# Performance work log

Hardware: AMD Instinct MI355X
Metric: run time of the kernel (lower is better)

The kernel has to match this reference:

```python
import jax, jax.numpy as jnp
import numpy as np

B, L, D = 8, 8192, 1024
M = L // 4  # target_ratio=4 -> exactly L/4 boundaries per batch row (enforced in setup_inputs)


@jax.custom_vjp
def ste(x):
    # Forward: ones_like(x). Backward: pass gradient straight through.
    return jnp.ones_like(x)

def _ste_fwd(x):
    return jnp.ones_like(x), None

def _ste_bwd(_, g):
    return (g,)

ste.defvjp(_ste_fwd, _ste_bwd)


def _ema_combine(c1, c2):
    # Linear recurrence h = a*h_prev + b as an associative op (matches the
    # Hillis-Steele doubling scan in the torch source exactly).
    a1, b1 = c1
    a2, b2 = c2
    return (a1 * a2, a2[..., None] * b1 + b2)


def setup_inputs() -> dict:
    key = jax.random.key(0)
    k1, k2, k3, k4, k5 = jax.random.split(key, 5)
    x = jax.random.normal(k1, (B, L, D), jnp.float32)
    residual = jax.random.normal(k2, (B, L, D), jnp.float32)
    prob = jax.random.uniform(k3, (B, L), jnp.float32)
    # exactly M=L//4 True positions per row (random locations) -> static M
    r = jax.random.uniform(k4, (B, L))
    sel = jnp.argsort(r, axis=1)[:, :M]
    token_mask = jnp.zeros((B, L), bool).at[jnp.arange(B)[:, None], sel].set(True)
    state = jax.random.normal(k5, (B, D), jnp.float32)
    return {"x": x, "residual": residual, "prob": prob,
            "token_mask": token_mask, "state": state}


def reference(x, residual, prob, token_mask, state):
    # ---- Tokenizer: compact selected positions to the front (stable order) ----
    counts = token_mask.sum(axis=1)                       # (B,)
    order = jnp.argsort(~token_mask, axis=1)[:, :M]       # stable: True positions first, in order
    chunked = jnp.take_along_axis(x, order[:, :, None], axis=1)      # (B, M, D)
    chunk_probs = jnp.take_along_axis(prob, order, axis=1)           # (B, M)
    valid = jnp.arange(M)[None, :] < counts[:, None]                  # (B, M)
    chunk_probs = chunk_probs * valid                     # padded slots -> 0 (new_zeros semantics)

    # ---- EMA scan over compacted chunks ----
    decay = jnp.clip(1.0 - chunk_probs, 0.0, 1.0)         # (B, M)
    b = (1.0 - decay)[..., None] * chunked                # (B, M, D)
    b = b.at[:, 0].add(decay[:, 0, None] * state)         # fold initial state into b[0]
    _, ema = jax.lax.associative_scan(_ema_combine, (decay, b), axis=1)
    ema = ema * valid[..., None]

    # ---- DeTokenizer: scatter-expand back to (B, L, D) ----
    chunk_idx = jnp.cumsum(token_mask.astype(jnp.int32), axis=1) - 1  # (B, L)
    valid_pos = chunk_idx >= 0
    ci = jnp.clip(chunk_idx, 0, M - 1)
    long_states = jnp.take_along_axis(ema, ci[:, :, None], axis=1)    # (B, L, D)
    long_states = long_states * valid_pos[..., None]

    coef = ste(jnp.maximum(1.0 - prob, prob))             # forward: ones; bwd: STE
    long_states = long_states * coef[..., None]

    output = residual + long_states                       # (B, L, D)

    # new_state = last valid EMA value per batch (or carried-over state if empty)
    last = jnp.clip(counts - 1, 0, M - 1)
    new_state = jnp.take_along_axis(ema, last[:, None, None], axis=1)[:, 0]
    new_state = jnp.where((counts > 0)[:, None], new_state, state)
    return output, new_state
```

## Files before the change

kernel.cpp:

```cpp
#include <hip/hip_runtime.h>
#include <stdint.h>
#include <stddef.h>

#define B_ 8
#define L_ 8192
#define D_ 1024
#define M_ 2048
#define D4_ (D_/4)
#define TROWS_ 256
#define NTILE_ (L_/TROWS_)
#define NBLK_ (B_*NTILE_)

typedef float f4 __attribute__((ext_vector_type(4)));

#define OFF_POS    ((size_t)0)
#define OFF_DEC    (OFF_POS  + (size_t)B_*M_*4)
#define OFF_A      (OFF_DEC  + (size_t)B_*M_*4)
#define OFF_CIT    (OFF_A    + (size_t)B_*NTILE_*4)
#define OFF_EZ     (OFF_CIT  + (size_t)B_*NTILE_*4)
#define OFF_HINIT  (OFF_EZ   + (size_t)B_*NTILE_*D_*4)
#define WS_TOTAL   (OFF_HINIT + (size_t)B_*NTILE_*D_*4)

__global__ __launch_bounds__(1024)
void compact_kernel(const void* __restrict__ mask_raw,
                    const float* __restrict__ prob,
                    int* __restrict__ pos,
                    float* __restrict__ dec,
                    int* __restrict__ ci_tile) {
    const int b = blockIdx.x;
    const int t = threadIdx.x;

    __shared__ int u8flag;
    if (t == 0) u8flag = 0;
    __syncthreads();
    {
        const uint32_t* mu = (const uint32_t*)mask_raw;
        uint32_t w0 = mu[t * 2], w1 = mu[t * 2 + 1];
        if (w0 > 1u || w1 > 1u) atomicOr(&u8flag, 1);
    }
    __syncthreads();
    const bool u8 = (u8flag != 0);

    int mv[8];
    const int base_l = t * 8;
    if (u8) {
        const uint8_t* mrow = (const uint8_t*)mask_raw + (size_t)b * L_;
        #pragma unroll
        for (int j = 0; j < 8; j++) mv[j] = mrow[base_l + j] ? 1 : 0;
    } else {
        const int* mrow = (const int*)mask_raw + (size_t)b * L_;
        #pragma unroll
        for (int j = 0; j < 8; j++) mv[j] = mrow[base_l + j] ? 1 : 0;
    }
    int tsum = 0;
    #pragma unroll
    for (int j = 0; j < 8; j++) tsum += mv[j];

    const int lane = t & 63, wid = t >> 6;
    int v = tsum;
    #pragma unroll
    for (int off = 1; off < 64; off <<= 1) {
        int n = __shfl_up(v, off, 64);
        if (lane >= off) v += n;
    }
    __shared__ int wsum[16];
    __shared__ int woff[16];
    if (lane == 63) wsum[wid] = v;
    __syncthreads();
    if (t < 16) {
        int acc = 0;
        for (int w = 0; w < t; w++) acc += wsum[w];
        woff[t] = acc;
    }
    __syncthreads();
    int run = (v - tsum) + woff[wid];

    const float* prow = prob + (size_t)b * L_;
    #pragma unroll
    for (int j = 0; j < 8; j++) {
        const int l = base_l + j;
        if (mv[j]) {
            float d = 1.0f - prow[l];
            d = fminf(fmaxf(d, 0.0f), 1.0f);
            pos[(size_t)b * M_ + run] = l;
            dec[(size_t)b * M_ + run] = d;
            run += 1;
        }
    }
    if ((t & 31) == 31) {
        const int k = (t + 1) >> 5;
        if (k < NTILE_) ci_tile[b * NTILE_ + k] = run - 1;
    }
}

__global__ __launch_bounds__(256)
void segend_kernel(const f4* __restrict__ x4,
                   const int* __restrict__ pos,
                   const float* __restrict__ dec,
                   const int* __restrict__ ci_tile,
                   f4* __restrict__ ez4,
                   float* __restrict__ Aseg) {
    const int blk = blockIdx.x;
    const int b = blk >> 5;
    const int k = blk & (NTILE_ - 1);
    const int t = threadIdx.x;

    const int mlo = (k == 0) ? 0 : ci_tile[b * NTILE_ + k] + 1;
    const int mhi = (k == NTILE_ - 1) ? (M_ - 1) : ci_tile[b * NTILE_ + k + 1];
    const int n = mhi - mlo + 1;

    __shared__ int   pl[TROWS_];
    __shared__ float dl[TROWS_];
    if (t < n) {
        pl[t] = pos[(size_t)b * M_ + mlo + t];
        dl[t] = dec[(size_t)b * M_ + mlo + t];
    }
    __syncthreads();

    f4 h = (f4)(0.0f);
    float A = 1.0f;
    if (n > 0) {
        const f4* xrow = x4 + (size_t)b * L_ * D4_;
        for (int g = 0; g < n; g += 8) {
            f4    xv[8];
            float dd[8];
            #pragma unroll
            for (int j = 0; j < 8; j++) {
                const int mm = g + j;
                const int mc = (mm < n) ? mm : 0;
                dd[j] = (mm < n) ? dl[mc] : 1.0f;
                xv[j] = xrow[(size_t)pl[mc] * D4_ + t];
            }
            #pragma unroll
            for (int j = 0; j < 8; j++) {
                h = dd[j] * h + (1.0f - dd[j]) * xv[j];
                A *= dd[j];
            }
        }
    }
    ez4[(size_t)blk * D4_ + t] = h;
    if (t == 0) Aseg[blk] = A;
}

__global__ __launch_bounds__(64)
void combine_kernel(const float* __restrict__ ez,
                    const float* __restrict__ Aseg,
                    const float* __restrict__ state,
                    float* __restrict__ hinit,
                    float* __restrict__ newstate) {
    const int b = blockIdx.x;
    const int ch = blockIdx.y * 64 + threadIdx.x;
    __shared__ float Al[NTILE_];
    if (threadIdx.x < NTILE_) Al[threadIdx.x] = Aseg[b * NTILE_ + threadIdx.x];
    __syncthreads();

    float c = state[(size_t)b * D_ + ch];
    for (int s0 = 0; s0 < NTILE_; s0 += 8) {
        float e[8];
        #pragma unroll
        for (int j = 0; j < 8; j++)
            e[j] = ez[((size_t)b * NTILE_ + s0 + j) * D_ + ch];
        #pragma unroll
        for (int j = 0; j < 8; j++) {
            hinit[((size_t)b * NTILE_ + s0 + j) * D_ + ch] = c;
            c = fmaf(Al[s0 + j], c, e[j]);
        }
    }
    newstate[(size_t)b * D_ + ch] = c;
}

__global__ __launch_bounds__(256)
void fused_kernel(const f4* __restrict__ x4,
                  const f4* __restrict__ res4,
                  const int* __restrict__ pos,
                  const float* __restrict__ dec,
                  const int* __restrict__ ci_tile,
                  const f4* __restrict__ hinit4,
                  f4* __restrict__ out4) {
    const int blk = blockIdx.x;
    const int b = blk >> 5;
    const int k = blk & (NTILE_ - 1);
    const int t = threadIdx.x;
    const int l0 = k * TROWS_;

    const int m0 = (k == 0) ? -1 : ci_tile[b * NTILE_ + k];

    __shared__ int   pl[TROWS_ + 2];
    __shared__ float dl[TROWS_ + 2];
    for (int i = t; i < TROWS_ + 2; i += 256) {
        const int mm = m0 + 1 + i;
        if (mm < M_) {
            pl[i] = pos[(size_t)b * M_ + mm];
            dl[i] = dec[(size_t)b * M_ + mm];
        } else {
            pl[i] = L_;
            dl[i] = 1.0f;
        }
    }
    __syncthreads();

    const f4* xrow = x4 + (size_t)b * L_ * D4_;

    f4 h = hinit4[(size_t)blk * D4_ + t];
    float live = (m0 >= 0) ? 1.0f : 0.0f;

    const f4* resrow = res4 + (size_t)b * L_ * D4_;
    f4*       outrow = out4 + (size_t)b * L_ * D4_;

    int mi = 0;
    int nextb = pl[0];
    int a0 = (pl[0] < L_) ? pl[0] : 0;
    int a1 = (pl[1] < L_) ? pl[1] : 0;
    f4 xn  = xrow[(size_t)a0 * D4_ + t];
    f4 xn2 = xrow[(size_t)a1 * D4_ + t];
    int l = l0;

    #define ADV(K, HH, LV)                                                \
        if (l + (K) == nextb) {                                           \
            const float d_ = dl[mi];                                      \
            h = d_ * h + (1.0f - d_) * xn;                                \
            live = 1.0f;                                                  \
            xn = xn2;                                                     \
            ++mi;                                                         \
            nextb = pl[mi];                                               \
            const int nr_ = (pl[mi + 1] < L_) ? pl[mi + 1] : 0;           \
            xn2 = xrow[(size_t)nr_ * D4_ + t];                            \
        }                                                                 \
        HH = h; LV = live;

    #define STORE4                                                        \
        {                                                                 \
            f4 h0, h1, h2, h3;                                            \
            float v0, v1, v2, v3;                                         \
            ADV(0, h0, v0); ADV(1, h1, v1); ADV(2, h2, v2); ADV(3, h3, v3);\
            __builtin_nontemporal_store(c0 + v0 * h0, outrow + (size_t)(l + 0) * D4_ + t); \
            __builtin_nontemporal_store(c1 + v1 * h1, outrow + (size_t)(l + 1) * D4_ + t); \
            __builtin_nontemporal_store(c2 + v2 * h2, outrow + (size_t)(l + 2) * D4_ + t); \
            __builtin_nontemporal_store(c3 + v3 * h3, outrow + (size_t)(l + 3) * D4_ + t); \
        }

    f4 c0 = __builtin_nontemporal_load(resrow + (size_t)(l + 0) * D4_ + t);
    f4 c1 = __builtin_nontemporal_load(resrow + (size_t)(l + 1) * D4_ + t);
    f4 c2 = __builtin_nontemporal_load(resrow + (size_t)(l + 2) * D4_ + t);
    f4 c3 = __builtin_nontemporal_load(resrow + (size_t)(l + 3) * D4_ + t);
    f4 c4 = __builtin_nontemporal_load(resrow + (size_t)(l + 4) * D4_ + t);
    f4 c5 = __builtin_nontemporal_load(resrow + (size_t)(l + 5) * D4_ + t);
    f4 c6 = __builtin_nontemporal_load(resrow + (size_t)(l + 6) * D4_ + t);
    f4 c7 = __builtin_nontemporal_load(resrow + (size_t)(l + 7) * D4_ + t);

    for (int g = 0; g < (TROWS_ / 4) - 2; ++g) {
        f4 n0 = __builtin_nontemporal_load(resrow + (size_t)(l +  8) * D4_ + t);
        f4 n1 = __builtin_nontemporal_load(resrow + (size_t)(l +  9) * D4_ + t);
        f4 n2 = __builtin_nontemporal_load(resrow + (size_t)(l + 10) * D4_ + t);
        f4 n3 = __builtin_nontemporal_load(resrow + (size_t)(l + 11) * D4_ + t);
        STORE4;
        c0 = c4; c1 = c5; c2 = c6; c3 = c7;
        c4 = n0; c5 = n1; c6 = n2; c7 = n3;
        l += 4;
    }
    STORE4;
    c0 = c4; c1 = c5; c2 = c6; c3 = c7;
    l += 4;
    STORE4;
    #undef STORE4
    #undef ADV
}

extern "C" void kernel_launch(void* const* d_in, const int* in_sizes, int n_in,
                              void* d_out, int out_size, void* d_ws, size_t ws_size,
                              hipStream_t stream) {
    const float* x        = (const float*)d_in[0];
    const float* residual = (const float*)d_in[1];
    const float* prob     = (const float*)d_in[2];
    const void*  mask     = d_in[3];
    const float* state    = (const float*)d_in[4];

    float* out       = (float*)d_out;
    float* new_state = out + (size_t)B_ * L_ * D_;

    if (ws_size < WS_TOTAL) return;

    char* ws = (char*)d_ws;
    int*   pos     = (int*)  (ws + OFF_POS);
    float* dec     = (float*)(ws + OFF_DEC);
    float* Aseg    = (float*)(ws + OFF_A);
    int*   ci_tile = (int*)  (ws + OFF_CIT);
    float* ez      = (float*)(ws + OFF_EZ);
    float* hinit   = (float*)(ws + OFF_HINIT);

    compact_kernel<<<B_, 1024, 0, stream>>>(mask, prob, pos, dec, ci_tile);

    segend_kernel<<<NBLK_, 256, 0, stream>>>(
        (const f4*)x, pos, dec, ci_tile, (f4*)ez, Aseg);

    combine_kernel<<<dim3(B_, 16), 64, 0, stream>>>(
        ez, Aseg, state, hinit, new_state);

    fused_kernel<<<NBLK_, 256, 0, stream>>>(
        (const f4*)x, (const f4*)residual, pos, dec, ci_tile,
        (const f4*)hinit, (f4*)out);
}
```

Measured before the change: 125.5 us.

## Fuse mask compaction into segend and fused kernels, drop compact launch

Removes the separate per-batch compaction kernel. Each tile block now does its own local prefix scan over its 256 mask entries to build the selected-position and decay lists in shared memory. Tile counts and liveness are passed through workspace, with liveness derived in the combine kernel. This drops one launch and a serial 8-block stage, at the cost of scanning the mask twice (once in segend, once in fused).

```diff
diff --git a/kernel.cpp b/kernel.cpp
--- a/kernel.cpp
+++ b/kernel.cpp
@@ -13,145 +13,108 @@
 
 typedef float f4 __attribute__((ext_vector_type(4)));
 
-#define OFF_POS    ((size_t)0)
-#define OFF_DEC    (OFF_POS  + (size_t)B_*M_*4)
-#define OFF_A      (OFF_DEC  + (size_t)B_*M_*4)
-#define OFF_CIT    (OFF_A    + (size_t)B_*NTILE_*4)
-#define OFF_EZ     (OFF_CIT  + (size_t)B_*NTILE_*4)
-#define OFF_HINIT  (OFF_EZ   + (size_t)B_*NTILE_*D_*4)
-#define WS_TOTAL   (OFF_HINIT + (size_t)B_*NTILE_*D_*4)
-
-__global__ __launch_bounds__(1024)
-void compact_kernel(const void* __restrict__ mask_raw,
-                    const float* __restrict__ prob,
-                    int* __restrict__ pos,
-                    float* __restrict__ dec,
-                    int* __restrict__ ci_tile) {
-    const int b = blockIdx.x;
-    const int t = threadIdx.x;
-
-    __shared__ int u8flag;
-    if (t == 0) u8flag = 0;
-    __syncthreads();
-    {
-        const uint32_t* mu = (const uint32_t*)mask_raw;
-        uint32_t w0 = mu[t * 2], w1 = mu[t * 2 + 1];
-        if (w0 > 1u || w1 > 1u) atomicOr(&u8flag, 1);
-    }
-    __syncthreads();
-    const bool u8 = (u8flag != 0);
-
-    int mv[8];
-    const int base_l = t * 8;
-    if (u8) {
-        const uint8_t* mrow = (const uint8_t*)mask_raw + (size_t)b * L_;
-        #pragma unroll
-        for (int j = 0; j < 8; j++) mv[j] = mrow[base_l + j] ? 1 : 0;
-    } else {
-        const int* mrow = (const int*)mask_raw + (size_t)b * L_;
-        #pragma unroll
-        for (int j = 0; j < 8; j++) mv[j] = mrow[base_l + j] ? 1 : 0;
-    }
-    int tsum = 0;
-    #pragma unroll
-    for (int j = 0; j < 8; j++) tsum += mv[j];
-
-    const int lane = t & 63, wid = t >> 6;
-    int v = tsum;
-    #pragma unroll
-    for (int off = 1; off < 64; off <<= 1) {
-        int n = __shfl_up(v, off, 64);
-        if (lane >= off) v += n;
-    }
-    __shared__ int wsum[16];
-    __shared__ int woff[16];
-    if (lane == 63) wsum[wid] = v;
-    __syncthreads();
-    if (t < 16) {
-        int acc = 0;
-        for (int w = 0; w < t; w++) acc += wsum[w];
-        woff[t] = acc;
-    }
-    __syncthreads();
-    int run = (v - tsum) + woff[wid];
-
-    const float* prow = prob + (size_t)b * L_;
-    #pragma unroll
-    for (int j = 0; j < 8; j++) {
-        const int l = base_l + j;
-        if (mv[j]) {
-            float d = 1.0f - prow[l];
-            d = fminf(fmaxf(d, 0.0f), 1.0f);
-            pos[(size_t)b * M_ + run] = l;
-            dec[(size_t)b * M_ + run] = d;
-            run += 1;
-        }
-    }
-    if ((t & 31) == 31) {
-        const int k = (t + 1) >> 5;
-        if (k < NTILE_) ci_tile[b * NTILE_ + k] = run - 1;
-    }
-}
+#define OFF_FLAG   ((size_t)0)
+#define OFF_A      ((size_t)256)
+#define OFF_CNT    (OFF_A    + (size_t)NBLK_*4)
+#define OFF_LIVE   (OFF_CNT  + (size_t)NBLK_*4)
+#define OFF_EZ     (OFF_LIVE + (size_t)NBLK_*4)
+#define OFF_HINIT  (OFF_EZ   + (size_t)NBLK_*D_*4)
+#define WS_TOTAL   (OFF_HINIT + (size_t)NBLK_*D_*4)
 
 __global__ __launch_bounds__(256)
 void segend_kernel(const f4* __restrict__ x4,
-                   const int* __restrict__ pos,
-                   const float* __restrict__ dec,
-                   const int* __restrict__ ci_tile,
+                   const float* __restrict__ prob,
+                   const void* __restrict__ mask_raw,
                    f4* __restrict__ ez4,
-                   float* __restrict__ Aseg) {
+                   float* __restrict__ Aseg,
+                   int* __restrict__ cnt,
+                   int* __restrict__ u8out) {
     const int blk = blockIdx.x;
     const int b = blk >> 5;
     const int k = blk & (NTILE_ - 1);
     const int t = threadIdx.x;
-
-    const int mlo = (k == 0) ? 0 : ci_tile[b * NTILE_ + k] + 1;
-    const int mhi = (k == NTILE_ - 1) ? (M_ - 1) : ci_tile[b * NTILE_ + k + 1];
-    const int n = mhi - mlo + 1;
-
-    __shared__ int   pl[TROWS_];
-    __shared__ float dl[TROWS_];
-    if (t < n) {
-        pl[t] = pos[(size_t)b * M_ + mlo + t];
-        dl[t] = dec[(size_t)b * M_ + mlo + t];
-    }
+    const int l0 = k * TROWS_;
+
+    __shared__ int   u8flag;
+    __shared__ int   wsum[4];
+    __shared__ int   pl[TROWS_ + 2];
+    __shared__ float dl[TROWS_ + 2];
+
+    if (t == 0) u8flag = 0;
+    __syncthreads();
+    {
+        const uint32_t* mu = (const uint32_t*)mask_raw;
+        uint32_t orv = 0;
+        #pragma unroll
+        for (int j = 0; j < 8; j++) orv |= mu[t * 8 + j];
+        if (orv > 1u) atomicOr(&u8flag, 1);
+    }
+    pl[t] = L_; dl[t] = 1.0f;
+    if (t < 2) { pl[TROWS_ + t] = L_; dl[TROWS_ + t] = 1.0f; }
+    __syncthreads();
+    const bool u8 = (u8flag != 0);
+    if (blk == 0 && t == 0) *u8out = u8 ? 1 : 0;
+
+    const int gl = b * L_ + l0 + t;
+    const int mv = u8 ? (((const uint8_t*)mask_raw)[gl] ? 1 : 0)
+                      : (((const int*)mask_raw)[gl] ? 1 : 0);
+    const float dv = fminf(fmaxf(1.0f - prob[gl], 0.0f), 1.0f);
+    const int lane = t & 63, wid = t >> 6;
+    int v = mv;
+    #pragma unroll
+    for (int off = 1; off < 64; off <<= 1) {
+        int nn = __shfl_up(v, off, 64);
+        if (lane >= off) v += nn;
+    }
+    if (lane == 63) wsum[wid] = v;
+    __syncthreads();
+    int acc = 0;
+    #pragma unroll
+    for (int w = 0; w < 4; w++) if (w < wid) acc += wsum[w];
+    const int n = wsum[0] + wsum[1] + wsum[2] + wsum[3];
+    const int excl = (v - mv) + acc;
+    if (mv) { pl[excl] = l0 + t; dl[excl] = dv; }
     __syncthreads();
 
     f4 h = (f4)(0.0f);
     float A = 1.0f;
-    if (n > 0) {
-        const f4* xrow = x4 + (size_t)b * L_ * D4_;
-        for (int g = 0; g < n; g += 8) {
-            f4    xv[8];
-            float dd[8];
-            #pragma unroll
-            for (int j = 0; j < 8; j++) {
-                const int mm = g + j;
-                const int mc = (mm < n) ? mm : 0;
-                dd[j] = (mm < n) ? dl[mc] : 1.0f;
-                xv[j] = xrow[(size_t)pl[mc] * D4_ + t];
-            }
-            #pragma unroll
-            for (int j = 0; j < 8; j++) {
-                h = dd[j] * h + (1.0f - dd[j]) * xv[j];
-                A *= dd[j];
-            }
+    const f4* xrow = x4 + (size_t)b * L_ * D4_;
+    for (int g = 0; g < n; g += 8) {
+        f4    xv[8];
+        float dd[8];
+        #pragma unroll
+        for (int j = 0; j < 8; j++) {
+            const int mm = g + j;
+            const int mc = (mm < n) ? mm : 0;
+            dd[j] = (mm < n) ? dl[mc] : 1.0f;
+            xv[j] = xrow[(size_t)pl[mc] * D4_ + t];
+        }
+        #pragma unroll
+        for (int j = 0; j < 8; j++) {
+            h = dd[j] * h + (1.0f - dd[j]) * xv[j];
+            A *= dd[j];
         }
     }
     ez4[(size_t)blk * D4_ + t] = h;
-    if (t == 0) Aseg[blk] = A;
+    if (t == 0) { Aseg[blk] = A; cnt[blk] = n; }
 }
 
 __global__ __launch_bounds__(64)
 void combine_kernel(const float* __restrict__ ez,
                     const float* __restrict__ Aseg,
+                    const int* __restrict__ cnt,
                     const float* __restrict__ state,
                     float* __restrict__ hinit,
+                    int* __restrict__ live,
                     float* __restrict__ newstate) {
     const int b = blockIdx.x;
     const int ch = blockIdx.y * 64 + threadIdx.x;
     __shared__ float Al[NTILE_];
-    if (threadIdx.x < NTILE_) Al[threadIdx.x] = Aseg[b * NTILE_ + threadIdx.x];
+    __shared__ int   Cl[NTILE_];
+    if (threadIdx.x < NTILE_) {
+        Al[threadIdx.x] = Aseg[b * NTILE_ + threadIdx.x];
+        Cl[threadIdx.x] = cnt[b * NTILE_ + threadIdx.x];
+    }
     __syncthreads();
 
     float c = state[(size_t)b * D_ + ch];
@@ -167,14 +130,22 @@
         }
     }
     newstate[(size_t)b * D_ + ch] = c;
+    if (blockIdx.y == 0 && threadIdx.x == 0) {
+        int cc = 0;
+        for (int kk = 0; kk < NTILE_; kk++) {
+            live[b * NTILE_ + kk] = (cc > 0) ? 1 : 0;
+            cc += Cl[kk];
+        }
+    }
 }
 
 __global__ __launch_bounds__(256)
 void fused_kernel(const f4* __restrict__ x4,
                   const f4* __restrict__ res4,
-                  const int* __restrict__ pos,
-                  const float* __restrict__ dec,
-                  const int* __restrict__ ci_tile,
+                  const float* __restrict__ prob,
+                  const void* __restrict__ mask_raw,
+                  const int* __restrict__ u8in,
+                  const int* __restrict__ liveA,
                   const f4* __restrict__ hinit4,
                   f4* __restrict__ out4) {
     const int blk = blockIdx.x;
@@ -183,26 +154,38 @@
     const int t = threadIdx.x;
     const int l0 = k * TROWS_;
 
-    const int m0 = (k == 0) ? -1 : ci_tile[b * NTILE_ + k];
-
+    __shared__ int   wsum[4];
     __shared__ int   pl[TROWS_ + 2];
     __shared__ float dl[TROWS_ + 2];
-    for (int i = t; i < TROWS_ + 2; i += 256) {
-        const int mm = m0 + 1 + i;
-        if (mm < M_) {
-            pl[i] = pos[(size_t)b * M_ + mm];
-            dl[i] = dec[(size_t)b * M_ + mm];
-        } else {
-            pl[i] = L_;
-            dl[i] = 1.0f;
-        }
-    }
+
+    pl[t] = L_; dl[t] = 1.0f;
+    if (t < 2) { pl[TROWS_ + t] = L_; dl[TROWS_ + t] = 1.0f; }
+    const bool u8 = (*u8in != 0);
+
+    const int gl = b * L_ + l0 + t;
+    const int mv = u8 ? (((const uint8_t*)mask_raw)[gl] ? 1 : 0)
+                      : (((const int*)mask_raw)[gl] ? 1 : 0);
+    const float dv = fminf(fmaxf(1.0f - prob[gl], 0.0f), 1.0f);
+    const int lane = t & 63, wid = t >> 6;
+    int v = mv;
+    #pragma unroll
+    for (int off = 1; off < 64; off <<= 1) {
+        int nn = __shfl_up(v, off, 64);
+        if (lane >= off) v += nn;
+    }
+    if (lane == 63) wsum[wid] = v;
+    __syncthreads();
+    int acc = 0;
+    #pragma unroll
+    for (int w = 0; w < 4; w++) if (w < wid) acc += wsum[w];
+    const int excl = (v - mv) + acc;
+    if (mv) { pl[excl] = l0 + t; dl[excl] = dv; }
     __syncthreads();
 
     const f4* xrow = x4 + (size_t)b * L_ * D4_;
 
     f4 h = hinit4[(size_t)blk * D4_ + t];
-    float live = (m0 >= 0) ? 1.0f : 0.0f;
+    float live = liveA[blk] ? 1.0f : 0.0f;
 
     const f4* resrow = res4 + (size_t)b * L_ * D4_;
     f4*       outrow = out4 + (size_t)b * L_ * D4_;
@@ -281,22 +264,20 @@
     if (ws_size < WS_TOTAL) return;
 
     char* ws = (char*)d_ws;
-    int*   pos     = (int*)  (ws + OFF_POS);
-    float* dec     = (float*)(ws + OFF_DEC);
-    float* Aseg    = (float*)(ws + OFF_A);
-    int*   ci_tile = (int*)  (ws + OFF_CIT);
-    float* ez      = (float*)(ws + OFF_EZ);
-    float* hinit   = (float*)(ws + OFF_HINIT);
-
-    compact_kernel<<<B_, 1024, 0, stream>>>(mask, prob, pos, dec, ci_tile);
+    int*   u8flag = (int*)  (ws + OFF_FLAG);
+    float* Aseg   = (float*)(ws + OFF_A);
+    int*   cnt    = (int*)  (ws + OFF_CNT);
+    int*   live   = (int*)  (ws + OFF_LIVE);
+    float* ez     = (float*)(ws + OFF_EZ);
+    float* hinit  = (float*)(ws + OFF_HINIT);
 
     segend_kernel<<<NBLK_, 256, 0, stream>>>(
-        (const f4*)x, pos, dec, ci_tile, (f4*)ez, Aseg);
+        (const f4*)x, prob, mask, (f4*)ez, Aseg, cnt, u8flag);
 
     combine_kernel<<<dim3(B_, 16), 64, 0, stream>>>(
-        ez, Aseg, state, hinit, new_state);
+        ez, Aseg, cnt, state, hinit, live, new_state);
 
     fused_kernel<<<NBLK_, 256, 0, stream>>>(
-        (const f4*)x, (const f4*)residual, pos, dec, ci_tile,
+        (const f4*)x, (const f4*)residual, prob, mask, u8flag, live,
         (const f4*)hinit, (f4*)out);
 }
```

Measured after the change: 120.9 us. 1.04x faster.
